# Kernel tuning notes

Hardware: AMD Instinct MI355X
Metric: run time of the kernel (lower is better)

The kernel has to match this reference:

```python
import jax, jax.numpy as jnp
import numpy as np

N, E, D = 50000, 600000, 128


def setup_inputs() -> dict:
    key = jax.random.key(0)
    ks = jax.random.split(key, 7)
    s = 1.0 / np.sqrt(D)
    return {
        "x": jax.random.normal(ks[0], (N, D), dtype=jnp.float32),
        "edge_index": jax.random.randint(ks[1], (2, E), 0, N, dtype=jnp.int64),
        "Wl1": jax.random.normal(ks[2], (D, D), dtype=jnp.float32) * s,
        "Wr1": jax.random.normal(ks[3], (D, D), dtype=jnp.float32) * s,
        "b1": jnp.zeros((D,), dtype=jnp.float32),
        "Wl2": jax.random.normal(ks[4], (D, D), dtype=jnp.float32) * s,
        "Wr2": jax.random.normal(ks[5], (D, D), dtype=jnp.float32) * s,
        "b2": jnp.zeros((D,), dtype=jnp.float32),
    }


def _sage_conv(h, edge_index, Wl, Wr, b):
    # PyG SAGEConv (mean aggr): out = lin_l(mean_{j in N(i)} h_j) + lin_r(h_i)
    src, dst = edge_index[0], edge_index[1]
    n = h.shape[0]
    msg = h[src]                                            # [E, D] gather
    agg = jax.ops.segment_sum(msg, dst, num_segments=n)     # [N, D] scatter-add
    cnt = jax.ops.segment_sum(jnp.ones((src.shape[0],), h.dtype), dst,
                              num_segments=n)               # in-degree
    agg = agg / jnp.maximum(cnt, 1.0)[:, None]              # mean (0 for isolated)
    return agg @ Wl + h @ Wr + b


def reference(x, edge_index, Wl1, Wr1, b1, Wl2, Wr2, b2):
    h = jax.nn.relu(_sage_conv(x, edge_index, Wl1, Wr1, b1))
    # F.dropout(p=0.5) is identity in eval mode (deterministic baseline)
    return _sage_conv(h, edge_index, Wl2, Wr2, b2)
```

## Files before the change

### kernel.cpp

```cpp
#include <hip/hip_runtime.h>

typedef unsigned int u32;
typedef unsigned short u16;
typedef __attribute__((ext_vector_type(8))) short bf16x8;
typedef __attribute__((ext_vector_type(4))) float f32x4;

__device__ __forceinline__ u32 f2bf(float f) {
  u32 x = __float_as_uint(f);
  return (x + 0x7fffu + ((x >> 16) & 1u)) >> 16;
}
__device__ __forceinline__ float bf2f(u16 u) {
  return __uint_as_float(((u32)u) << 16);
}
__device__ __forceinline__ void addbf8(float* a, uint4 v) {
  a[0] += bf2f((u16)v.x); a[1] += bf2f((u16)(v.x >> 16));
  a[2] += bf2f((u16)v.y); a[3] += bf2f((u16)(v.y >> 16));
  a[4] += bf2f((u16)v.z); a[5] += bf2f((u16)(v.z >> 16));
  a[6] += bf2f((u16)v.w); a[7] += bf2f((u16)(v.w >> 16));
}

__global__ void setup_kernel(const float* __restrict__ Wl1, const float* __restrict__ Wr1,
                             const float* __restrict__ Wl2, const float* __restrict__ Wr2,
                             u16* __restrict__ G1, u16* __restrict__ G2,
                             int* __restrict__ cnt, int n) {
  int b = blockIdx.x;
  if (b < 256) {
    const float* Wl = (b < 128) ? Wl1 : Wl2;
    const float* Wr = (b < 128) ? Wr1 : Wr2;
    u16* G = (b < 128) ? G1 : G2;
    int id = (b & 127) * 256 + threadIdx.x;
    int c = id >> 7;
    int k = id & 127;
    const float* W = (c < 128) ? Wl : Wr;
    float v = W[k * 128 + (c & 127)];
    G[c * 128 + (k ^ ((c & 7) << 3))] = (u16)f2bf(v);
  } else {
    int i = (b - 256) * 256 + threadIdx.x;
    if (i < n) cnt[i] = 0;
  }
}

__global__ void hist_kernel(const int* __restrict__ dst, int* __restrict__ cnt, int E) {
  int e = blockIdx.x * blockDim.x + threadIdx.x;
  if (e < E) atomicAdd(&cnt[dst[e]], 1);
}

#define SCAN_CHUNK 2048

__global__ __launch_bounds__(256) void scan_sums(const int* __restrict__ cnt,
                                                 int* __restrict__ bsum, int n) {
  __shared__ int red[256];
  int t = threadIdx.x;
  int base = blockIdx.x * SCAN_CHUNK + t * 8;
  int s = 0;
#pragma unroll
  for (int i = 0; i < 8; ++i) {
    int idx = base + i;
    if (idx < n) s += cnt[idx];
  }
  red[t] = s;
  __syncthreads();
  for (int off = 128; off > 0; off >>= 1) {
    if (t < off) red[t] += red[t + off];
    __syncthreads();
  }
  if (t == 0) bsum[blockIdx.x] = red[0];
}

__global__ __launch_bounds__(256) void scan_apply(
    const int* __restrict__ cnt, const int* __restrict__ bsum, int nb,
    int* __restrict__ row_ptr, int* __restrict__ fill_pos,
    float* __restrict__ inv_cnt, int n) {
  __shared__ int sc[256];
  __shared__ int base_s;
  int t = threadIdx.x;
  if (t == 0) {
    int run = 0;
    int bid = blockIdx.x;
    int base = 0;
    for (int i = 0; i < nb; ++i) {
      if (i == bid) base = run;
      run += bsum[i];
    }
    base_s = base;
    if (bid == 0) row_ptr[n] = run;
  }
  int chunk_base = blockIdx.x * SCAN_CHUNK + t * 8;
  int v[8];
  int s = 0;
#pragma unroll
  for (int i = 0; i < 8; ++i) {
    int idx = chunk_base + i;
    v[i] = (idx < n) ? cnt[idx] : 0;
    s += v[i];
  }
  sc[t] = s;
  __syncthreads();
  for (int off = 1; off < 256; off <<= 1) {
    int add = (t >= off) ? sc[t - off] : 0;
    __syncthreads();
    sc[t] += add;
    __syncthreads();
  }
  int run = base_s + ((t > 0) ? sc[t - 1] : 0);
#pragma unroll
  for (int i = 0; i < 8; ++i) {
    int idx = chunk_base + i;
    if (idx < n) {
      row_ptr[idx] = run;
      fill_pos[idx] = run;
      inv_cnt[idx] = 1.0f / (float)max(v[i], 1);
      run += v[i];
    }
  }
}

template <int IN_BF16>
__device__ __forceinline__ void gemm_tiles(const void* in_, const u16* __restrict__ G,
                                           const float* __restrict__ bias,
                                           u16* __restrict__ yl, u16* __restrict__ yr,
                                           int n, uint4* lds4, int gb) {
  char* As = (char*)lds4;
  char* Bt = (char*)lds4 + 16384;
  const int t = threadIdx.x;
  const int lane = t & 63;
  const int wave = t >> 6;
  const int wr = wave >> 1;
  const int wc = wave & 1;
  const int lhi = lane >> 4;
  const int llo = lane & 15;

  {
    const uint4* gbp = (const uint4*)G;
    uint4* lb = lds4 + 1024;
#pragma unroll
    for (int i = 0; i < 16; ++i) lb[i * 256 + t] = gbp[i * 256 + t];
  }

  const int ntiles = (n + 63) / 64;
#pragma unroll 1
  for (int tile = gb * 2; tile < ntiles && tile < gb * 2 + 2; ++tile) {
    const int row0 = tile * 64;
    __syncthreads();
#pragma unroll
    for (int i = 0; i < 4; ++i) {
      int g = t + i * 256;
      int r = g >> 4;
      int gc = g & 15;
      int row = row0 + r;
      uint4 pk = {0u, 0u, 0u, 0u};
      if (row < n) {
        if (IN_BF16) {
          pk = *(const uint4*)((const u16*)in_ + (size_t)row * 128 + gc * 8);
        } else {
          const float4* pp = (const float4*)((const float*)in_ + (size_t)row * 128 + gc * 8);
          float4 v0 = pp[0], v1 = pp[1];
          pk.x = f2bf(v0.x) | (f2bf(v0.y) << 16);
          pk.y = f2bf(v0.z) | (f2bf(v0.w) << 16);
          pk.z = f2bf(v1.x) | (f2bf(v1.y) << 16);
          pk.w = f2bf(v1.z) | (f2bf(v1.w) << 16);
        }
      }
      *(uint4*)(As + r * 256 + ((gc * 16) ^ ((r & 7) << 4))) = pk;
    }
    __syncthreads();

    f32x4 acc[2][8];
#pragma unroll
    for (int fr = 0; fr < 2; ++fr)
#pragma unroll
      for (int fc = 0; fc < 8; ++fc) acc[fr][fc] = {0.f, 0.f, 0.f, 0.f};

#pragma unroll
    for (int ks = 0; ks < 4; ++ks) {
      const int kbyte = ks * 64 + lhi * 16;
      bf16x8 a[2], bb[8];
#pragma unroll
      for (int fr = 0; fr < 2; ++fr) {
        int r = wr * 32 + fr * 16 + llo;
        a[fr] = *(const bf16x8*)(As + r * 256 + (kbyte ^ ((r & 7) << 4)));
      }
#pragma unroll
      for (int fc = 0; fc < 8; ++fc) {
        int c = wc * 128 + fc * 16 + llo;
        bb[fc] = *(const bf16x8*)(Bt + c * 256 + (kbyte ^ ((c & 7) << 4)));
      }
#pragma unroll
      for (int fr = 0; fr < 2; ++fr)
#pragma unroll
        for (int fc = 0; fc < 8; ++fc)
          acc[fr][fc] = __builtin_amdgcn_mfma_f32_16x16x32_bf16(a[fr], bb[fc], acc[fr][fc], 0, 0, 0);
    }

#pragma unroll 1
    for (int ph = 0; ph < 2; ++ph) {
      __syncthreads();
      if (wc == ph) {
        const float* bp = bias;
#pragma unroll
        for (int fc = 0; fc < 8; ++fc) {
          int cc = fc * 16 + llo;
          float bv = (ph == 1) ? bp[cc] : 0.0f;
#pragma unroll
          for (int fr = 0; fr < 2; ++fr) {
#pragma unroll
            for (int i = 0; i < 4; ++i) {
              int row = wr * 32 + fr * 16 + lhi * 4 + i;
              *(u16*)(As + row * 256 + ((cc * 2) ^ (lhi << 5))) =
                  (u16)f2bf(acc[fr][fc][i] + bv);
            }
          }
        }
      }
      __syncthreads();
      u16* outp = (ph == 0) ? yl : yr;
#pragma unroll
      for (int j = 0; j < 4; ++j) {
        int idx = t + j * 256;
        int row = idx >> 4;
        int cb = (idx & 15) * 16;
        int grow = row0 + row;
        if (grow < n) {
          uint4 v = *(const uint4*)(As + row * 256 + (cb ^ (((row >> 2) & 3) << 5)));
          *(uint4*)((char*)(outp + (size_t)grow * 128) + cb) = v;
        }
      }
    }
  }
}

__global__ __launch_bounds__(256, 2) void gemm1_fill_kernel(
    const float* __restrict__ x, const u16* __restrict__ G1, const float* __restrict__ b1,
    u16* __restrict__ yl, u16* __restrict__ yr, int n,
    const int* __restrict__ src, const int* __restrict__ dst,
    int* __restrict__ fill_pos, int* __restrict__ colv, int E, int GB) {
  __shared__ uint4 lds4[5120];
  if ((int)blockIdx.x < GB) {
    gemm_tiles<0>(x, G1, b1, yl, yr, n, lds4, blockIdx.x);
  } else {
    int base = ((int)blockIdx.x - GB) * 1024 + threadIdx.x;
    int dd[4], ss[4], pos[4];
#pragma unroll
    for (int j = 0; j < 4; ++j) {
      int e = base + j * 256;
      if (e < E) { dd[j] = dst[e]; ss[j] = src[e]; }
    }
#pragma unroll
    for (int j = 0; j < 4; ++j) {
      int e = base + j * 256;
      if (e < E) pos[j] = atomicAdd(&fill_pos[dd[j]], 1);
    }
#pragma unroll
    for (int j = 0; j < 4; ++j) {
      int e = base + j * 256;
      if (e < E) colv[pos[j]] = ss[j];
    }
  }
}

template <int IN_BF16>
__global__ __launch_bounds__(256, 2) void gemm_kernel(
    const void* __restrict__ in_, const u16* __restrict__ G, const float* __restrict__ bias,
    u16* __restrict__ yl, u16* __restrict__ yr, int n) {
  __shared__ uint4 lds4[5120];
  gemm_tiles<IN_BF16>(in_, G, bias, yl, yr, n, lds4, blockIdx.x);
}

template <int RELU, int OUT_BF16>
__global__ __launch_bounds__(256) void agg_kernel(
    const u16* __restrict__ yl, const u16* __restrict__ yr,
    const int* __restrict__ row_ptr, const int* __restrict__ colv,
    const float* __restrict__ invc, void* __restrict__ out_, int n) {
  int node = blockIdx.x * 16 + (threadIdx.x >> 4);
  if (node >= n) return;
  int sl = threadIdx.x & 15;
  int beg = row_ptr[node], end = row_ptr[node + 1];
  uint4 rv = *(const uint4*)(yr + (size_t)node * 128 + sl * 8);
  float s = invc[node];
  float a[8] = {0.f, 0.f, 0.f, 0.f, 0.f, 0.f, 0.f, 0.f};
  for (int e0 = beg; e0 < end; e0 += 8) {
    int m = end - e0;
    if (m > 8) m = 8;
    uint4 v0, v1, v2, v3, v4, v5, v6, v7;
    if (0 < m) v0 = *(const uint4*)(yl + (size_t)colv[e0 + 0] * 128 + sl * 8);
    if (1 < m) v1 = *(const uint4*)(yl + (size_t)colv[e0 + 1] * 128 + sl * 8);
    if (2 < m) v2 = *(const uint4*)(yl + (size_t)colv[e0 + 2] * 128 + sl * 8);
    if (3 < m) v3 = *(const uint4*)(yl + (size_t)colv[e0 + 3] * 128 + sl * 8);
    if (4 < m) v4 = *(const uint4*)(yl + (size_t)colv[e0 + 4] * 128 + sl * 8);
    if (5 < m) v5 = *(const uint4*)(yl + (size_t)colv[e0 + 5] * 128 + sl * 8);
    if (6 < m) v6 = *(const uint4*)(yl + (size_t)colv[e0 + 6] * 128 + sl * 8);
    if (7 < m) v7 = *(const uint4*)(yl + (size_t)colv[e0 + 7] * 128 + sl * 8);
    if (0 < m) addbf8(a, v0);
    if (1 < m) addbf8(a, v1);
    if (2 < m) addbf8(a, v2);
    if (3 < m) addbf8(a, v3);
    if (4 < m) addbf8(a, v4);
    if (5 < m) addbf8(a, v5);
    if (6 < m) addbf8(a, v6);
    if (7 < m) addbf8(a, v7);
  }
  float r[8];
  r[0] = bf2f((u16)rv.x); r[1] = bf2f((u16)(rv.x >> 16));
  r[2] = bf2f((u16)rv.y); r[3] = bf2f((u16)(rv.y >> 16));
  r[4] = bf2f((u16)rv.z); r[5] = bf2f((u16)(rv.z >> 16));
  r[6] = bf2f((u16)rv.w); r[7] = bf2f((u16)(rv.w >> 16));
  float o[8];
#pragma unroll
  for (int j = 0; j < 8; ++j) {
    o[j] = a[j] * s + r[j];
    if (RELU) o[j] = fmaxf(o[j], 0.f);
  }
  if (OUT_BF16) {
    uint4 pk;
    pk.x = f2bf(o[0]) | (f2bf(o[1]) << 16);
    pk.y = f2bf(o[2]) | (f2bf(o[3]) << 16);
    pk.z = f2bf(o[4]) | (f2bf(o[5]) << 16);
    pk.w = f2bf(o[6]) | (f2bf(o[7]) << 16);
    *(uint4*)((u16*)out_ + (size_t)node * 128 + sl * 8) = pk;
  } else {
    float4 q0 = {o[0], o[1], o[2], o[3]};
    float4 q1 = {o[4], o[5], o[6], o[7]};
    float* op = (float*)out_ + (size_t)node * 128 + sl * 8;
    *(float4*)op = q0;
    *(float4*)(op + 4) = q1;
  }
}

extern "C" void kernel_launch(void* const* d_in, const int* in_sizes, int n_in,
                              void* d_out, int out_size, void* d_ws, size_t ws_size,
                              hipStream_t stream) {
  const float* x = (const float*)d_in[0];
  const int* ei = (const int*)d_in[1];
  const float* Wl1 = (const float*)d_in[2];
  const float* Wr1 = (const float*)d_in[3];
  const float* b1 = (const float*)d_in[4];
  const float* Wl2 = (const float*)d_in[5];
  const float* Wr2 = (const float*)d_in[6];
  const float* b2 = (const float*)d_in[7];

  const int N = in_sizes[0] / 128;
  const int E = in_sizes[1] / 2;
  const int* srcv = ei;
  const int* dstv = ei + E;

  char* ws = (char*)d_ws;
  u16* yl = (u16*)ws;       ws += (size_t)N * 128 * 2;
  u16* yr = (u16*)ws;       ws += (size_t)N * 128 * 2;
  u16* hbf = (u16*)ws;      ws += (size_t)N * 128 * 2;
  u16* G1 = (u16*)ws;       ws += 256 * 128 * 2;
  u16* G2 = (u16*)ws;       ws += 256 * 128 * 2;
  int* colv = (int*)ws;     ws += (size_t)E * 4;
  int* row_ptr = (int*)ws;  ws += ((size_t)N + 64) * 4;
  int* fill_pos = (int*)ws; ws += (size_t)N * 4;
  int* cnt = (int*)ws;      ws += (size_t)N * 4;
  float* invc = (float*)ws; ws += (size_t)N * 4;
  int* bsum = (int*)ws;     ws += 256 * 4;

  const int nsb = (N + SCAN_CHUNK - 1) / SCAN_CHUNK;
  const int ntiles = (N + 63) / 64;
  const int GB = (ntiles + 1) / 2;
  const int FB = (E + 1023) / 1024;

  setup_kernel<<<256 + (N + 255) / 256, 256, 0, stream>>>(Wl1, Wr1, Wl2, Wr2, G1, G2, cnt, N);
  hist_kernel<<<(E + 255) / 256, 256, 0, stream>>>(dstv, cnt, E);
  scan_sums<<<nsb, 256, 0, stream>>>(cnt, bsum, N);
  scan_apply<<<nsb, 256, 0, stream>>>(cnt, bsum, nsb, row_ptr, fill_pos, invc, N);
  gemm1_fill_kernel<<<GB + FB, 256, 0, stream>>>(x, G1, b1, yl, yr, N,
                                                 srcv, dstv, fill_pos, colv, E, GB);
  agg_kernel<1, 1><<<(N + 15) / 16, 256, 0, stream>>>(yl, yr, row_ptr, colv, invc, hbf, N);
  gemm_kernel<1><<<GB, 256, 0, stream>>>(hbf, G2, b2, yl, yr, N);
  agg_kernel<0, 0><<<(N + 15) / 16, 256, 0, stream>>>(yl, yr, row_ptr, colv, invc, d_out, N);
}
```

Measured before the change: 164.2 us.

## Keep weight fragments in registers and shrink GEMM tiles to 32 rows

The GEMM no longer stages the full 256x128 bf16 weight matrix in LDS. Each wave now loads its 64-column slice of B directly into registers, and the weight swizzle is dropped. The tile shrinks to 32 rows and the output goes through a single 32x256 LDS staging buffer written in one phase instead of two. This cuts LDS use from 80KB to 24KB so occupancy can rise to 3 blocks per SM, and it uses a grid-stride tile loop. The cost is higher register pressure from 16 bf16x8 B fragments per thread, and each block still handles only about two tiles, so per-block weight loads are not amortized much.

```diff
diff --git a/kernel.cpp b/kernel.cpp
--- a/kernel.cpp
+++ b/kernel.cpp
@@ -32,8 +32,7 @@
     int c = id >> 7;
     int k = id & 127;
     const float* W = (c < 128) ? Wl : Wr;
-    float v = W[k * 128 + (c & 127)];
-    G[c * 128 + (k ^ ((c & 7) << 3))] = (u16)f2bf(v);
+    G[c * 128 + k] = (u16)f2bf(W[k * 128 + (c & 127)]);
   } else {
     int i = (b - 256) * 256 + threadIdx.x;
     if (i < n) cnt[i] = 0;
@@ -119,31 +118,33 @@
 __device__ __forceinline__ void gemm_tiles(const void* in_, const u16* __restrict__ G,
                                            const float* __restrict__ bias,
                                            u16* __restrict__ yl, u16* __restrict__ yr,
-                                           int n, uint4* lds4, int gb) {
+                                           int n, uint4* lds4, int gb, int nbg) {
   char* As = (char*)lds4;
-  char* Bt = (char*)lds4 + 16384;
+  char* Cs = (char*)lds4 + 8192;
   const int t = threadIdx.x;
   const int lane = t & 63;
   const int wave = t >> 6;
-  const int wr = wave >> 1;
-  const int wc = wave & 1;
   const int lhi = lane >> 4;
   const int llo = lane & 15;
 
-  {
-    const uint4* gbp = (const uint4*)G;
-    uint4* lb = lds4 + 1024;
-#pragma unroll
-    for (int i = 0; i < 16; ++i) lb[i * 256 + t] = gbp[i * 256 + t];
-  }
-
-  const int ntiles = (n + 63) / 64;
+  bf16x8 breg[4][4];
+  float bvv[4];
+#pragma unroll
+  for (int fc = 0; fc < 4; ++fc) {
+    int c = wave * 64 + fc * 16 + llo;
+    bvv[fc] = (c >= 128) ? bias[c - 128] : 0.0f;
+#pragma unroll
+    for (int ks = 0; ks < 4; ++ks)
+      breg[fc][ks] = *(const bf16x8*)(G + (size_t)c * 128 + ks * 32 + lhi * 8);
+  }
+
+  const int ntiles = (n + 31) / 32;
 #pragma unroll 1
-  for (int tile = gb * 2; tile < ntiles && tile < gb * 2 + 2; ++tile) {
-    const int row0 = tile * 64;
-    __syncthreads();
-#pragma unroll
-    for (int i = 0; i < 4; ++i) {
+  for (int tile = gb; tile < ntiles; tile += nbg) {
+    const int row0 = tile * 32;
+    __syncthreads();
+#pragma unroll
+    for (int i = 0; i < 2; ++i) {
       int g = t + i * 256;
       int r = g >> 4;
       int gc = g & 15;
@@ -165,78 +166,65 @@
     }
     __syncthreads();
 
-    f32x4 acc[2][8];
+    f32x4 acc[2][4];
 #pragma unroll
     for (int fr = 0; fr < 2; ++fr)
 #pragma unroll
-      for (int fc = 0; fc < 8; ++fc) acc[fr][fc] = {0.f, 0.f, 0.f, 0.f};
+      for (int fc = 0; fc < 4; ++fc) acc[fr][fc] = {0.f, 0.f, 0.f, 0.f};
 
 #pragma unroll
     for (int ks = 0; ks < 4; ++ks) {
       const int kbyte = ks * 64 + lhi * 16;
-      bf16x8 a[2], bb[8];
+      bf16x8 a[2];
 #pragma unroll
       for (int fr = 0; fr < 2; ++fr) {
-        int r = wr * 32 + fr * 16 + llo;
+        int r = fr * 16 + llo;
         a[fr] = *(const bf16x8*)(As + r * 256 + (kbyte ^ ((r & 7) << 4)));
       }
 #pragma unroll
-      for (int fc = 0; fc < 8; ++fc) {
-        int c = wc * 128 + fc * 16 + llo;
-        bb[fc] = *(const bf16x8*)(Bt + c * 256 + (kbyte ^ ((c & 7) << 4)));
-      }
-#pragma unroll
       for (int fr = 0; fr < 2; ++fr)
 #pragma unroll
-        for (int fc = 0; fc < 8; ++fc)
-          acc[fr][fc] = __builtin_amdgcn_mfma_f32_16x16x32_bf16(a[fr], bb[fc], acc[fr][fc], 0, 0, 0);
-    }
-
-#pragma unroll 1
-    for (int ph = 0; ph < 2; ++ph) {
-      __syncthreads();
-      if (wc == ph) {
-        const float* bp = bias;
-#pragma unroll
-        for (int fc = 0; fc < 8; ++fc) {
-          int cc = fc * 16 + llo;
-          float bv = (ph == 1) ? bp[cc] : 0.0f;
-#pragma unroll
-          for (int fr = 0; fr < 2; ++fr) {
-#pragma unroll
-            for (int i = 0; i < 4; ++i) {
-              int row = wr * 32 + fr * 16 + lhi * 4 + i;
-              *(u16*)(As + row * 256 + ((cc * 2) ^ (lhi << 5))) =
-                  (u16)f2bf(acc[fr][fc][i] + bv);
-            }
-          }
+        for (int fc = 0; fc < 4; ++fc)
+          acc[fr][fc] = __builtin_amdgcn_mfma_f32_16x16x32_bf16(a[fr], breg[fc][ks], acc[fr][fc], 0, 0, 0);
+    }
+
+#pragma unroll
+    for (int fc = 0; fc < 4; ++fc) {
+      int colb = (wave * 64 + fc * 16 + llo) * 2;
+#pragma unroll
+      for (int fr = 0; fr < 2; ++fr) {
+#pragma unroll
+        for (int i = 0; i < 4; ++i) {
+          int row = fr * 16 + lhi * 4 + i;
+          *(u16*)(Cs + row * 512 + (colb ^ (lhi << 5))) =
+              (u16)f2bf(acc[fr][fc][i] + bvv[fc]);
         }
       }
-      __syncthreads();
-      u16* outp = (ph == 0) ? yl : yr;
-#pragma unroll
-      for (int j = 0; j < 4; ++j) {
-        int idx = t + j * 256;
-        int row = idx >> 4;
-        int cb = (idx & 15) * 16;
-        int grow = row0 + row;
-        if (grow < n) {
-          uint4 v = *(const uint4*)(As + row * 256 + (cb ^ (((row >> 2) & 3) << 5)));
-          *(uint4*)((char*)(outp + (size_t)grow * 128) + cb) = v;
-        }
+    }
+    __syncthreads();
+#pragma unroll
+    for (int j = 0; j < 4; ++j) {
+      int idx = t + j * 256;
+      int row = idx >> 5;
+      int gc = idx & 31;
+      int grow = row0 + row;
+      if (grow < n) {
+        uint4 v = *(const uint4*)(Cs + row * 512 + ((gc * 16) ^ (((row >> 2) & 3) << 5)));
+        u16* outp = (gc < 16) ? yl : yr;
+        *(uint4*)(outp + (size_t)grow * 128 + (gc & 15) * 8) = v;
       }
     }
   }
 }
 
-__global__ __launch_bounds__(256, 2) void gemm1_fill_kernel(
+__global__ __launch_bounds__(256, 3) void gemm1_fill_kernel(
     const float* __restrict__ x, const u16* __restrict__ G1, const float* __restrict__ b1,
     u16* __restrict__ yl, u16* __restrict__ yr, int n,
     const int* __restrict__ src, const int* __restrict__ dst,
     int* __restrict__ fill_pos, int* __restrict__ colv, int E, int GB) {
-  __shared__ uint4 lds4[5120];
+  __shared__ uint4 lds4[1536];
   if ((int)blockIdx.x < GB) {
-    gemm_tiles<0>(x, G1, b1, yl, yr, n, lds4, blockIdx.x);
+    gemm_tiles<0>(x, G1, b1, yl, yr, n, lds4, blockIdx.x, GB);
   } else {
     int base = ((int)blockIdx.x - GB) * 1024 + threadIdx.x;
     int dd[4], ss[4], pos[4];
@@ -259,11 +247,11 @@
 }
 
 template <int IN_BF16>
-__global__ __launch_bounds__(256, 2) void gemm_kernel(
+__global__ __launch_bounds__(256, 3) void gemm_kernel(
     const void* __restrict__ in_, const u16* __restrict__ G, const float* __restrict__ bias,
     u16* __restrict__ yl, u16* __restrict__ yr, int n) {
-  __shared__ uint4 lds4[5120];
-  gemm_tiles<IN_BF16>(in_, G, bias, yl, yr, n, lds4, blockIdx.x);
+  __shared__ uint4 lds4[1536];
+  gemm_tiles<IN_BF16>(in_, G, bias, yl, yr, n, lds4, blockIdx.x, gridDim.x);
 }
 
 template <int RELU, int OUT_BF16>
@@ -357,7 +345,7 @@
   int* bsum = (int*)ws;     ws += 256 * 4;
 
   const int nsb = (N + SCAN_CHUNK - 1) / SCAN_CHUNK;
-  const int ntiles = (N + 63) / 64;
+  const int ntiles = (N + 31) / 32;
   const int GB = (ntiles + 1) / 2;
   const int FB = (E + 1023) / 1024;
 
```

New measurement: 177.8 us. 8.3% more time.

## Fuse layer-1 aggregation into layer-2 GEMM, removing intermediate h buffer

Applied to the files above, without the earlier changes.

Layer-1 neighbor-mean aggregation plus ReLU now runs inside the layer-2 GEMM kernel. Each block aggregates its 64-row tile straight into LDS and feeds the MFMA stage from there, so the bf16 hidden activations no longer round-trip through global memory and one launch goes away. The cost is lower gather parallelism. Only GB blocks (about 391) run the irregular gather, with a non-unrolled row loop inside a GEMM-sized block, so latency hiding may suffer. Separate yl2/yr2 buffers avoid overwriting layer-1 outputs.

```diff
diff --git a/kernel.cpp b/kernel.cpp
--- a/kernel.cpp
+++ b/kernel.cpp
@@ -115,20 +115,85 @@
   }
 }
 
-template <int IN_BF16>
-__device__ __forceinline__ void gemm_tiles(const void* in_, const u16* __restrict__ G,
-                                           const float* __restrict__ bias,
-                                           u16* __restrict__ yl, u16* __restrict__ yr,
-                                           int n, uint4* lds4, int gb) {
-  char* As = (char*)lds4;
-  char* Bt = (char*)lds4 + 16384;
-  const int t = threadIdx.x;
+__device__ __forceinline__ void mfma_and_store(
+    const float* __restrict__ bias, u16* __restrict__ yl, u16* __restrict__ yr,
+    int n, int row0, char* As, char* Bt, int t) {
   const int lane = t & 63;
   const int wave = t >> 6;
   const int wr = wave >> 1;
   const int wc = wave & 1;
   const int lhi = lane >> 4;
   const int llo = lane & 15;
+
+  f32x4 acc[2][8];
+#pragma unroll
+  for (int fr = 0; fr < 2; ++fr)
+#pragma unroll
+    for (int fc = 0; fc < 8; ++fc) acc[fr][fc] = {0.f, 0.f, 0.f, 0.f};
+
+#pragma unroll
+  for (int ks = 0; ks < 4; ++ks) {
+    const int kbyte = ks * 64 + lhi * 16;
+    bf16x8 a[2], bb[8];
+#pragma unroll
+    for (int fr = 0; fr < 2; ++fr) {
+      int r = wr * 32 + fr * 16 + llo;
+      a[fr] = *(const bf16x8*)(As + r * 256 + (kbyte ^ ((r & 7) << 4)));
+    }
+#pragma unroll
+    for (int fc = 0; fc < 8; ++fc) {
+      int c = wc * 128 + fc * 16 + llo;
+      bb[fc] = *(const bf16x8*)(Bt + c * 256 + (kbyte ^ ((c & 7) << 4)));
+    }
+#pragma unroll
+    for (int fr = 0; fr < 2; ++fr)
+#pragma unroll
+      for (int fc = 0; fc < 8; ++fc)
+        acc[fr][fc] = __builtin_amdgcn_mfma_f32_16x16x32_bf16(a[fr], bb[fc], acc[fr][fc], 0, 0, 0);
+  }
+
+#pragma unroll 1
+  for (int ph = 0; ph < 2; ++ph) {
+    __syncthreads();
+    if (wc == ph) {
+#pragma unroll
+      for (int fc = 0; fc < 8; ++fc) {
+        int cc = fc * 16 + llo;
+        float bv = (ph == 1) ? bias[cc] : 0.0f;
+#pragma unroll
+        for (int fr = 0; fr < 2; ++fr) {
+#pragma unroll
+          for (int i = 0; i < 4; ++i) {
+            int row = wr * 32 + fr * 16 + lhi * 4 + i;
+            *(u16*)(As + row * 256 + ((cc * 2) ^ (lhi << 5))) =
+                (u16)f2bf(acc[fr][fc][i] + bv);
+          }
+        }
+      }
+    }
+    __syncthreads();
+    u16* outp = (ph == 0) ? yl : yr;
+#pragma unroll
+    for (int j = 0; j < 4; ++j) {
+      int idx = t + j * 256;
+      int row = idx >> 4;
+      int cb = (idx & 15) * 16;
+      int grow = row0 + row;
+      if (grow < n) {
+        uint4 v = *(const uint4*)(As + row * 256 + (cb ^ (((row >> 2) & 3) << 5)));
+        *(uint4*)((char*)(outp + (size_t)grow * 128) + cb) = v;
+      }
+    }
+  }
+}
+
+__device__ __forceinline__ void gemm_tiles_l1(const float* in_, const u16* __restrict__ G,
+                                              const float* __restrict__ bias,
+                                              u16* __restrict__ yl, u16* __restrict__ yr,
+                                              int n, uint4* lds4, int gb) {
+  char* As = (char*)lds4;
+  char* Bt = (char*)lds4 + 16384;
+  const int t = threadIdx.x;
 
   {
     const uint4* gbp = (const uint4*)G;
@@ -150,82 +215,17 @@
       int row = row0 + r;
       uint4 pk = {0u, 0u, 0u, 0u};
       if (row < n) {
-        if (IN_BF16) {
-          pk = *(const uint4*)((const u16*)in_ + (size_t)row * 128 + gc * 8);
-        } else {
-          const float4* pp = (const float4*)((const float*)in_ + (size_t)row * 128 + gc * 8);
-          float4 v0 = pp[0], v1 = pp[1];
-          pk.x = f2bf(v0.x) | (f2bf(v0.y) << 16);
-          pk.y = f2bf(v0.z) | (f2bf(v0.w) << 16);
-          pk.z = f2bf(v1.x) | (f2bf(v1.y) << 16);
-          pk.w = f2bf(v1.z) | (f2bf(v1.w) << 16);
-        }
+        const float4* pp = (const float4*)(in_ + (size_t)row * 128 + gc * 8);
+        float4 v0 = pp[0], v1 = pp[1];
+        pk.x = f2bf(v0.x) | (f2bf(v0.y) << 16);
+        pk.y = f2bf(v0.z) | (f2bf(v0.w) << 16);
+        pk.z = f2bf(v1.x) | (f2bf(v1.y) << 16);
+        pk.w = f2bf(v1.z) | (f2bf(v1.w) << 16);
       }
       *(uint4*)(As + r * 256 + ((gc * 16) ^ ((r & 7) << 4))) = pk;
     }
     __syncthreads();
-
-    f32x4 acc[2][8];
-#pragma unroll
-    for (int fr = 0; fr < 2; ++fr)
-#pragma unroll
-      for (int fc = 0; fc < 8; ++fc) acc[fr][fc] = {0.f, 0.f, 0.f, 0.f};
-
-#pragma unroll
-    for (int ks = 0; ks < 4; ++ks) {
-      const int kbyte = ks * 64 + lhi * 16;
-      bf16x8 a[2], bb[8];
-#pragma unroll
-      for (int fr = 0; fr < 2; ++fr) {
-        int r = wr * 32 + fr * 16 + llo;
-        a[fr] = *(const bf16x8*)(As + r * 256 + (kbyte ^ ((r & 7) << 4)));
-      }
-#pragma unroll
-      for (int fc = 0; fc < 8; ++fc) {
-        int c = wc * 128 + fc * 16 + llo;
-        bb[fc] = *(const bf16x8*)(Bt + c * 256 + (kbyte ^ ((c & 7) << 4)));
-      }
-#pragma unroll
-      for (int fr = 0; fr < 2; ++fr)
-#pragma unroll
-        for (int fc = 0; fc < 8; ++fc)
-          acc[fr][fc] = __builtin_amdgcn_mfma_f32_16x16x32_bf16(a[fr], bb[fc], acc[fr][fc], 0, 0, 0);
-    }
-
-#pragma unroll 1
-    for (int ph = 0; ph < 2; ++ph) {
-      __syncthreads();
-      if (wc == ph) {
-        const float* bp = bias;
-#pragma unroll
-        for (int fc = 0; fc < 8; ++fc) {
-          int cc = fc * 16 + llo;
-          float bv = (ph == 1) ? bp[cc] : 0.0f;
-#pragma unroll
-          for (int fr = 0; fr < 2; ++fr) {
-#pragma unroll
-            for (int i = 0; i < 4; ++i) {
-              int row = wr * 32 + fr * 16 + lhi * 4 + i;
-              *(u16*)(As + row * 256 + ((cc * 2) ^ (lhi << 5))) =
-                  (u16)f2bf(acc[fr][fc][i] + bv);
-            }
-          }
-        }
-      }
-      __syncthreads();
-      u16* outp = (ph == 0) ? yl : yr;
-#pragma unroll
-      for (int j = 0; j < 4; ++j) {
-        int idx = t + j * 256;
-        int row = idx >> 4;
-        int cb = (idx & 15) * 16;
-        int grow = row0 + row;
-        if (grow < n) {
-          uint4 v = *(const uint4*)(As + row * 256 + (cb ^ (((row >> 2) & 3) << 5)));
-          *(uint4*)((char*)(outp + (size_t)grow * 128) + cb) = v;
-        }
-      }
-    }
+    mfma_and_store(bias, yl, yr, n, row0, As, Bt, t);
   }
 }
 
@@ -236,7 +236,7 @@
     int* __restrict__ fill_pos, int* __restrict__ colv, int E, int GB) {
   __shared__ uint4 lds4[5120];
   if ((int)blockIdx.x < GB) {
-    gemm_tiles<0>(x, G1, b1, yl, yr, n, lds4, blockIdx.x);
+    gemm_tiles_l1(x, G1, b1, yl, yr, n, lds4, blockIdx.x);
   } else {
     int base = ((int)blockIdx.x - GB) * 1024 + threadIdx.x;
     int dd[4], ss[4], pos[4];
@@ -258,19 +258,87 @@
   }
 }
 
-template <int IN_BF16>
-__global__ __launch_bounds__(256, 2) void gemm_kernel(
-    const void* __restrict__ in_, const u16* __restrict__ G, const float* __restrict__ bias,
-    u16* __restrict__ yl, u16* __restrict__ yr, int n) {
+__global__ __launch_bounds__(256, 2) void agg_gemm_kernel(
+    const u16* __restrict__ yl1, const u16* __restrict__ yr1,
+    const int* __restrict__ row_ptr, const int* __restrict__ colv,
+    const float* __restrict__ invc, const u16* __restrict__ G2,
+    const float* __restrict__ b2, u16* __restrict__ yl2, u16* __restrict__ yr2,
+    int n) {
   __shared__ uint4 lds4[5120];
-  gemm_tiles<IN_BF16>(in_, G, bias, yl, yr, n, lds4, blockIdx.x);
-}
-
-template <int RELU, int OUT_BF16>
-__global__ __launch_bounds__(256) void agg_kernel(
+  char* As = (char*)lds4;
+  char* Bt = (char*)lds4 + 16384;
+  const int t = threadIdx.x;
+  const int grp = t >> 4;
+  const int sl = t & 15;
+
+  {
+    const uint4* gbp = (const uint4*)G2;
+    uint4* lb = lds4 + 1024;
+#pragma unroll
+    for (int i = 0; i < 16; ++i) lb[i * 256 + t] = gbp[i * 256 + t];
+  }
+
+  const int ntiles = (n + 63) / 64;
+#pragma unroll 1
+  for (int tile = blockIdx.x * 2; tile < ntiles && tile < blockIdx.x * 2 + 2; ++tile) {
+    const int row0 = tile * 64;
+    __syncthreads();
+#pragma unroll 1
+    for (int rr = 0; rr < 4; ++rr) {
+      int r = grp + rr * 16;
+      int node = row0 + r;
+      uint4 pk = {0u, 0u, 0u, 0u};
+      if (node < n) {
+        int beg = row_ptr[node], end = row_ptr[node + 1];
+        uint4 rv = *(const uint4*)(yr1 + (size_t)node * 128 + sl * 8);
+        float s = invc[node];
+        float a[8] = {0.f, 0.f, 0.f, 0.f, 0.f, 0.f, 0.f, 0.f};
+        for (int e0 = beg; e0 < end; e0 += 8) {
+          int m = end - e0;
+          if (m > 8) m = 8;
+          uint4 v0, v1, v2, v3, v4, v5, v6, v7;
+          if (0 < m) v0 = *(const uint4*)(yl1 + (size_t)colv[e0 + 0] * 128 + sl * 8);
+          if (1 < m) v1 = *(const uint4*)(yl1 + (size_t)colv[e0 + 1] * 128 + sl * 8);
+          if (2 < m) v2 = *(const uint4*)(yl1 + (size_t)colv[e0 + 2] * 128 + sl * 8);
+          if (3 < m) v3 = *(const uint4*)(yl1 + (size_t)colv[e0 + 3] * 128 + sl * 8);
+          if (4 < m) v4 = *(const uint4*)(yl1 + (size_t)colv[e0 + 4] * 128 + sl * 8);
+          if (5 < m) v5 = *(const uint4*)(yl1 + (size_t)colv[e0 + 5] * 128 + sl * 8);
+          if (6 < m) v6 = *(const uint4*)(yl1 + (size_t)colv[e0 + 6] * 128 + sl * 8);
+          if (7 < m) v7 = *(const uint4*)(yl1 + (size_t)colv[e0 + 7] * 128 + sl * 8);
+          if (0 < m) addbf8(a, v0);
+          if (1 < m) addbf8(a, v1);
+          if (2 < m) addbf8(a, v2);
+          if (3 < m) addbf8(a, v3);
+          if (4 < m) addbf8(a, v4);
+          if (5 < m) addbf8(a, v5);
+          if (6 < m) addbf8(a, v6);
+          if (7 < m) addbf8(a, v7);
+        }
+        float o[8];
+        o[0] = fmaxf(a[0] * s + bf2f((u16)rv.x), 0.f);
+        o[1] = fmaxf(a[1] * s + bf2f((u16)(rv.x >> 16)), 0.f);
+        o[2] = fmaxf(a[2] * s + bf2f((u16)rv.y), 0.f);
+        o[3] = fmaxf(a[3] * s + bf2f((u16)(rv.y >> 16)), 0.f);
+        o[4] = fmaxf(a[4] * s + bf2f((u16)rv.z), 0.f);
+        o[5] = fmaxf(a[5] * s + bf2f((u16)(rv.z >> 16)), 0.f);
+        o[6] = fmaxf(a[6] * s + bf2f((u16)rv.w), 0.f);
+        o[7] = fmaxf(a[7] * s + bf2f((u16)(rv.w >> 16)), 0.f);
+        pk.x = f2bf(o[0]) | (f2bf(o[1]) << 16);
+        pk.y = f2bf(o[2]) | (f2bf(o[3]) << 16);
+        pk.z = f2bf(o[4]) | (f2bf(o[5]) << 16);
+        pk.w = f2bf(o[6]) | (f2bf(o[7]) << 16);
+      }
+      *(uint4*)(As + r * 256 + ((sl * 16) ^ ((r & 7) << 4))) = pk;
+    }
+    __syncthreads();
+    mfma_and_store(b2, yl2, yr2, n, row0, As, Bt, t);
+  }
+}
+
+__global__ __launch_bounds__(256) void agg_kernel_final(
     const u16* __restrict__ yl, const u16* __restrict__ yr,
     const int* __restrict__ row_ptr, const int* __restrict__ colv,
-    const float* __restrict__ invc, void* __restrict__ out_, int n) {
+    const float* __restrict__ invc, float* __restrict__ out, int n) {
   int node = blockIdx.x * 16 + (threadIdx.x >> 4);
   if (node >= n) return;
   int sl = threadIdx.x & 15;
@@ -306,24 +374,12 @@
   r[6] = bf2f((u16)rv.w); r[7] = bf2f((u16)(rv.w >> 16));
   float o[8];
 #pragma unroll
-  for (int j = 0; j < 8; ++j) {
-    o[j] = a[j] * s + r[j];
-    if (RELU) o[j] = fmaxf(o[j], 0.f);
-  }
-  if (OUT_BF16) {
-    uint4 pk;
-    pk.x = f2bf(o[0]) | (f2bf(o[1]) << 16);
-    pk.y = f2bf(o[2]) | (f2bf(o[3]) << 16);
-    pk.z = f2bf(o[4]) | (f2bf(o[5]) << 16);
-    pk.w = f2bf(o[6]) | (f2bf(o[7]) << 16);
-    *(uint4*)((u16*)out_ + (size_t)node * 128 + sl * 8) = pk;
-  } else {
-    float4 q0 = {o[0], o[1], o[2], o[3]};
-    float4 q1 = {o[4], o[5], o[6], o[7]};
-    float* op = (float*)out_ + (size_t)node * 128 + sl * 8;
-    *(float4*)op = q0;
-    *(float4*)(op + 4) = q1;
-  }
+  for (int j = 0; j < 8; ++j) o[j] = a[j] * s + r[j];
+  float4 q0 = {o[0], o[1], o[2], o[3]};
+  float4 q1 = {o[4], o[5], o[6], o[7]};
+  float* op = out + (size_t)node * 128 + sl * 8;
+  *(float4*)op = q0;
+  *(float4*)(op + 4) = q1;
 }
 
 extern "C" void kernel_launch(void* const* d_in, const int* in_sizes, int n_in,
@@ -344,9 +400,10 @@
   const int* dstv = ei + E;
 
   char* ws = (char*)d_ws;
-  u16* yl = (u16*)ws;       ws += (size_t)N * 128 * 2;
-  u16* yr = (u16*)ws;       ws += (size_t)N * 128 * 2;
-  u16* hbf = (u16*)ws;      ws += (size_t)N * 128 * 2;
+  u16* yl1 = (u16*)ws;      ws += (size_t)N * 128 * 2;
+  u16* yr1 = (u16*)ws;      ws += (size_t)N * 128 * 2;
+  u16* yl2 = (u16*)ws;      ws += (size_t)N * 128 * 2;
+  u16* yr2 = (u16*)ws;      ws += (size_t)N * 128 * 2;
   u16* G1 = (u16*)ws;       ws += 256 * 128 * 2;
   u16* G2 = (u16*)ws;       ws += 256 * 128 * 2;
   int* colv = (int*)ws;     ws += (size_t)E * 4;
@@ -365,9 +422,10 @@
   hist_kernel<<<(E + 255) / 256, 256, 0, stream>>>(dstv, cnt, E);
   scan_sums<<<nsb, 256, 0, stream>>>(cnt, bsum, N);
   scan_apply<<<nsb, 256, 0, stream>>>(cnt, bsum, nsb, row_ptr, fill_pos, invc, N);
-  gemm1_fill_kernel<<<GB + FB, 256, 0, stream>>>(x, G1, b1, yl, yr, N,
+  gemm1_fill_kernel<<<GB + FB, 256, 0, stream>>>(x, G1, b1, yl1, yr1, N,
                                                  srcv, dstv, fill_pos, colv, E, GB);
-  agg_kernel<1, 1><<<(N + 15) / 16, 256, 0, stream>>>(yl, yr, row_ptr, colv, invc, hbf, N);
-  gemm_kernel<1><<<GB, 256, 0, stream>>>(hbf, G2, b2, yl, yr, N);
-  agg_kernel<0, 0><<<(N + 15) / 16, 256, 0, stream>>>(yl, yr, row_ptr, colv, invc, d_out, N);
-}
+  agg_gemm_kernel<<<GB, 256, 0, stream>>>(yl1, yr1, row_ptr, colv, invc,
+                                          G2, b2, yl2, yr2, N);
+  agg_kernel_final<<<(N + 15) / 16, 256, 0, stream>>>(yl2, yr2, row_ptr, colv, invc,
+                                                      (float*)d_out, N);
+}
```

Result: slower. 187.4 us (+14.2%).

## Split GEMM blocks into per-tile half-output blocks to raise parallelism

Applied to the files above, without the earlier changes.

Each GEMM block previously handled two 64-row tiles and both Wl and Wr output halves (256 columns). Now each block handles one 64-row tile and one half (Wl or Wr), so there are four times as many blocks, each with less LDS and fewer accumulators, which allows 3 blocks per CU. The trade-off is that every input tile is now loaded and converted twice, once per half, which adds redundant global reads and fp32-to-bf16 work.

```diff
diff --git a/kernel.cpp b/kernel.cpp
--- a/kernel.cpp
+++ b/kernel.cpp
@@ -116,12 +116,12 @@
 }
 
 template <int IN_BF16>
-__device__ __forceinline__ void gemm_tiles(const void* in_, const u16* __restrict__ G,
-                                           const float* __restrict__ bias,
-                                           u16* __restrict__ yl, u16* __restrict__ yr,
-                                           int n, uint4* lds4, int gb) {
+__device__ __forceinline__ void gemm_halfblock(const void* in_, const u16* __restrict__ G,
+                                               const float* __restrict__ bias,
+                                               u16* __restrict__ yl, u16* __restrict__ yr,
+                                               int n, uint4* lds4, int tile, int half) {
   char* As = (char*)lds4;
-  char* Bt = (char*)lds4 + 16384;
+  char* Bs = (char*)lds4 + 16384;
   const int t = threadIdx.x;
   const int lane = t & 63;
   const int wave = t >> 6;
@@ -129,114 +129,105 @@
   const int wc = wave & 1;
   const int lhi = lane >> 4;
   const int llo = lane & 15;
+  const int row0 = tile * 64;
 
   {
-    const uint4* gbp = (const uint4*)G;
+    const uint4* gbp = (const uint4*)(G + (size_t)half * 128 * 128);
     uint4* lb = lds4 + 1024;
 #pragma unroll
-    for (int i = 0; i < 16; ++i) lb[i * 256 + t] = gbp[i * 256 + t];
-  }
-
-  const int ntiles = (n + 63) / 64;
-#pragma unroll 1
-  for (int tile = gb * 2; tile < ntiles && tile < gb * 2 + 2; ++tile) {
-    const int row0 = tile * 64;
-    __syncthreads();
-#pragma unroll
-    for (int i = 0; i < 4; ++i) {
-      int g = t + i * 256;
-      int r = g >> 4;
-      int gc = g & 15;
-      int row = row0 + r;
-      uint4 pk = {0u, 0u, 0u, 0u};
-      if (row < n) {
-        if (IN_BF16) {
-          pk = *(const uint4*)((const u16*)in_ + (size_t)row * 128 + gc * 8);
-        } else {
-          const float4* pp = (const float4*)((const float*)in_ + (size_t)row * 128 + gc * 8);
-          float4 v0 = pp[0], v1 = pp[1];
-          pk.x = f2bf(v0.x) | (f2bf(v0.y) << 16);
-          pk.y = f2bf(v0.z) | (f2bf(v0.w) << 16);
-          pk.z = f2bf(v1.x) | (f2bf(v1.y) << 16);
-          pk.w = f2bf(v1.z) | (f2bf(v1.w) << 16);
+    for (int i = 0; i < 8; ++i) lb[i * 256 + t] = gbp[i * 256 + t];
+  }
+#pragma unroll
+  for (int i = 0; i < 4; ++i) {
+    int g = t + i * 256;
+    int r = g >> 4;
+    int gc = g & 15;
+    int row = row0 + r;
+    uint4 pk = {0u, 0u, 0u, 0u};
+    if (row < n) {
+      if (IN_BF16) {
+        pk = *(const uint4*)((const u16*)in_ + (size_t)row * 128 + gc * 8);
+      } else {
+        const float4* pp = (const float4*)((const float*)in_ + (size_t)row * 128 + gc * 8);
+        float4 v0 = pp[0], v1 = pp[1];
+        pk.x = f2bf(v0.x) | (f2bf(v0.y) << 16);
+        pk.y = f2bf(v0.z) | (f2bf(v0.w) << 16);
+        pk.z = f2bf(v1.x) | (f2bf(v1.y) << 16);
+        pk.w = f2bf(v1.z) | (f2bf(v1.w) << 16);
+      }
+    }
+    *(uint4*)(As + r * 256 + ((gc * 16) ^ ((r & 7) << 4))) = pk;
+  }
+  __syncthreads();
+
+  f32x4 acc[2][4];
+#pragma unroll
+  for (int fr = 0; fr < 2; ++fr)
+#pragma unroll
+    for (int fc = 0; fc < 4; ++fc) acc[fr][fc] = {0.f, 0.f, 0.f, 0.f};
+
+#pragma unroll
+  for (int ks = 0; ks < 4; ++ks) {
+    const int kbyte = ks * 64 + lhi * 16;
+    bf16x8 a[2], bb[4];
+#pragma unroll
+    for (int fr = 0; fr < 2; ++fr) {
+      int r = wr * 32 + fr * 16 + llo;
+      a[fr] = *(const bf16x8*)(As + r * 256 + (kbyte ^ ((r & 7) << 4)));
+    }
+#pragma unroll
+    for (int fc = 0; fc < 4; ++fc) {
+      int lc = wc * 64 + fc * 16 + llo;
+      bb[fc] = *(const bf16x8*)(Bs + lc * 256 + (kbyte ^ ((lc & 7) << 4)));
+    }
+#pragma unroll
+    for (int fr = 0; fr < 2; ++fr)
+#pragma unroll
+      for (int fc = 0; fc < 4; ++fc)
+        acc[fr][fc] = __builtin_amdgcn_mfma_f32_16x16x32_bf16(a[fr], bb[fc], acc[fr][fc], 0, 0, 0);
+  }
+
+  __syncthreads();
+  {
+    float bv_base = 0.0f;
+#pragma unroll
+    for (int fc = 0; fc < 4; ++fc) {
+      int cc = wc * 64 + fc * 16 + llo;
+      float bv = half ? bias[cc] : bv_base;
+#pragma unroll
+      for (int fr = 0; fr < 2; ++fr) {
+#pragma unroll
+        for (int i = 0; i < 4; ++i) {
+          int row = wr * 32 + fr * 16 + lhi * 4 + i;
+          *(u16*)(As + row * 256 + ((cc * 2) ^ (lhi << 5))) =
+              (u16)f2bf(acc[fr][fc][i] + bv);
         }
       }
-      *(uint4*)(As + r * 256 + ((gc * 16) ^ ((r & 7) << 4))) = pk;
-    }
-    __syncthreads();
-
-    f32x4 acc[2][8];
-#pragma unroll
-    for (int fr = 0; fr < 2; ++fr)
-#pragma unroll
-      for (int fc = 0; fc < 8; ++fc) acc[fr][fc] = {0.f, 0.f, 0.f, 0.f};
-
-#pragma unroll
-    for (int ks = 0; ks < 4; ++ks) {
-      const int kbyte = ks * 64 + lhi * 16;
-      bf16x8 a[2], bb[8];
-#pragma unroll
-      for (int fr = 0; fr < 2; ++fr) {
-        int r = wr * 32 + fr * 16 + llo;
-        a[fr] = *(const bf16x8*)(As + r * 256 + (kbyte ^ ((r & 7) << 4)));
-      }
-#pragma unroll
-      for (int fc = 0; fc < 8; ++fc) {
-        int c = wc * 128 + fc * 16 + llo;
-        bb[fc] = *(const bf16x8*)(Bt + c * 256 + (kbyte ^ ((c & 7) << 4)));
-      }
-#pragma unroll
-      for (int fr = 0; fr < 2; ++fr)
-#pragma unroll
-        for (int fc = 0; fc < 8; ++fc)
-          acc[fr][fc] = __builtin_amdgcn_mfma_f32_16x16x32_bf16(a[fr], bb[fc], acc[fr][fc], 0, 0, 0);
-    }
-
-#pragma unroll 1
-    for (int ph = 0; ph < 2; ++ph) {
-      __syncthreads();
-      if (wc == ph) {
-        const float* bp = bias;
-#pragma unroll
-        for (int fc = 0; fc < 8; ++fc) {
-          int cc = fc * 16 + llo;
-          float bv = (ph == 1) ? bp[cc] : 0.0f;
-#pragma unroll
-          for (int fr = 0; fr < 2; ++fr) {
-#pragma unroll
-            for (int i = 0; i < 4; ++i) {
-              int row = wr * 32 + fr * 16 + lhi * 4 + i;
-              *(u16*)(As + row * 256 + ((cc * 2) ^ (lhi << 5))) =
-                  (u16)f2bf(acc[fr][fc][i] + bv);
-            }
-          }
-        }
-      }
-      __syncthreads();
-      u16* outp = (ph == 0) ? yl : yr;
-#pragma unroll
-      for (int j = 0; j < 4; ++j) {
-        int idx = t + j * 256;
-        int row = idx >> 4;
-        int cb = (idx & 15) * 16;
-        int grow = row0 + row;
-        if (grow < n) {
-          uint4 v = *(const uint4*)(As + row * 256 + (cb ^ (((row >> 2) & 3) << 5)));
-          *(uint4*)((char*)(outp + (size_t)grow * 128) + cb) = v;
-        }
-      }
-    }
-  }
-}
-
-__global__ __launch_bounds__(256, 2) void gemm1_fill_kernel(
+    }
+  }
+  __syncthreads();
+  u16* outp = half ? yr : yl;
+#pragma unroll
+  for (int j = 0; j < 4; ++j) {
+    int idx = t + j * 256;
+    int row = idx >> 4;
+    int cb = (idx & 15) * 16;
+    int grow = row0 + row;
+    if (grow < n) {
+      uint4 v = *(const uint4*)(As + row * 256 + (cb ^ (((row >> 2) & 3) << 5)));
+      *(uint4*)((char*)(outp + (size_t)grow * 128) + cb) = v;
+    }
+  }
+}
+
+__global__ __launch_bounds__(256, 3) void gemm1_fill_kernel(
     const float* __restrict__ x, const u16* __restrict__ G1, const float* __restrict__ b1,
     u16* __restrict__ yl, u16* __restrict__ yr, int n,
     const int* __restrict__ src, const int* __restrict__ dst,
     int* __restrict__ fill_pos, int* __restrict__ colv, int E, int GB) {
-  __shared__ uint4 lds4[5120];
+  __shared__ uint4 lds4[3072];
   if ((int)blockIdx.x < GB) {
-    gemm_tiles<0>(x, G1, b1, yl, yr, n, lds4, blockIdx.x);
+    gemm_halfblock<0>(x, G1, b1, yl, yr, n, lds4, blockIdx.x >> 1, blockIdx.x & 1);
   } else {
     int base = ((int)blockIdx.x - GB) * 1024 + threadIdx.x;
     int dd[4], ss[4], pos[4];
@@ -259,11 +250,11 @@
 }
 
 template <int IN_BF16>
-__global__ __launch_bounds__(256, 2) void gemm_kernel(
+__global__ __launch_bounds__(256, 3) void gemm_kernel(
     const void* __restrict__ in_, const u16* __restrict__ G, const float* __restrict__ bias,
     u16* __restrict__ yl, u16* __restrict__ yr, int n) {
-  __shared__ uint4 lds4[5120];
-  gemm_tiles<IN_BF16>(in_, G, bias, yl, yr, n, lds4, blockIdx.x);
+  __shared__ uint4 lds4[3072];
+  gemm_halfblock<IN_BF16>(in_, G, bias, yl, yr, n, lds4, blockIdx.x >> 1, blockIdx.x & 1);
 }
 
 template <int RELU, int OUT_BF16>
@@ -358,7 +349,7 @@
 
   const int nsb = (N + SCAN_CHUNK - 1) / SCAN_CHUNK;
   const int ntiles = (N + 63) / 64;
-  const int GB = (ntiles + 1) / 2;
+  const int GB = ntiles * 2;
   const int FB = (E + 1023) / 1024;
 
   setup_kernel<<<256 + (N + 255) / 256, 256, 0, stream>>>(Wl1, Wr1, Wl2, Wr2, G1, G2, cnt, N);
```

Result: slower. 174.6 us (+6.4%).
